# Optimization experiments

Hardware: AMD Instinct MI355X
Metric: run time of the kernel (lower is better)

Reference implementation:

```python
import jax, jax.numpy as jnp
import numpy as np

N = 100000   # nodes of target type
N1 = 80000   # nodes of second type
D = 128      # raw feature dim
H = 64       # hidden dim
C = 16       # n_classes
G = 3        # number of graphs (metapaths)
E = 1000000  # edges per graph
K = 20       # neighbors per node for NS branch
LP_LAYERS = 3


def setup_inputs() -> dict:
    key = jax.random.key(0)
    ks = jax.random.split(key, 24)
    f = lambda i, shape: jax.random.normal(ks[i], shape, dtype=jnp.float32)
    feats0 = f(0, (N, D))
    feats1 = f(1, (N1, D))
    W0 = f(2, (D, H)) * 0.05
    b0 = jnp.zeros((H,), jnp.float32)
    W1 = f(3, (D, H)) * 0.05
    b1 = jnp.zeros((H,), jnp.float32)
    Wp = f(4, (D, H)) * 0.05
    Wcls = f(5, (H, C)) * 0.05
    bcls = jnp.zeros((C,), jnp.float32)
    alpha = f(6, (N, 1)) * 0.1
    attention = f(7, (N, G, 1))
    y = jax.random.randint(ks[8], (N,), 0, C)
    labels_one_hot = jax.nn.one_hot(y, C, dtype=jnp.float32)
    byte_idx_train = jax.random.bernoulli(ks[9], 0.3, (N, 1))
    label_init = jnp.full((N, C), 1.0 / C, jnp.float32)
    nei_idx = jax.random.randint(ks[10], (N, K), 0, N1, dtype=jnp.int32)
    src0 = jax.random.randint(ks[11], (E,), 0, N, dtype=jnp.int32)
    dst0 = jax.random.randint(ks[12], (E,), 0, N, dtype=jnp.int32)
    src1 = jax.random.randint(ks[13], (E,), 0, N, dtype=jnp.int32)
    dst1 = jax.random.randint(ks[14], (E,), 0, N, dtype=jnp.int32)
    src2 = jax.random.randint(ks[15], (E,), 0, N, dtype=jnp.int32)
    dst2 = jax.random.randint(ks[16], (E,), 0, N, dtype=jnp.int32)
    return dict(feats0=feats0, feats1=feats1, W0=W0, b0=b0, W1=W1, b1=b1,
                Wp=Wp, Wcls=Wcls, bcls=bcls, alpha=alpha, attention=attention,
                labels_one_hot=labels_one_hot, label_init=label_init,
                byte_idx_train=byte_idx_train, nei_idx=nei_idx,
                src0=src0, dst0=dst0, src1=src1, dst1=dst1, src2=src2, dst2=dst2)


def _propagate(fp, h, src, dst, n):
    # edge attention: dot-product score of projected feats, softmax per dst
    s = jnp.sum(fp[src] * fp[dst], axis=-1) / np.sqrt(fp.shape[-1])   # [E]
    m = jax.ops.segment_max(s, dst, num_segments=n)                   # [N]
    e = jnp.exp(s - jnp.where(jnp.isfinite(m), m, 0.0)[dst])          # [E]
    denom = jax.ops.segment_sum(e, dst, num_segments=n)               # [N]
    att = e / (denom[dst] + 1e-16)                                    # [E]
    return jax.ops.segment_sum(att[:, None] * h[src], dst, num_segments=n)


def reference(feats0, feats1, W0, b0, W1, b1, Wp, Wcls, bcls, alpha, attention,
              labels_one_hot, label_init, byte_idx_train, nei_idx,
              src0, dst0, src1, dst1, src2, dst2):
    n = label_init.shape[0]
    masked = byte_idx_train.astype(jnp.float32)          # [N,1]
    masked_label = 1.0 - masked                          # (~mask).float()
    masked_onehot = labels_one_hot * masked              # clamp train labels

    fp = feats0 @ Wp                                     # shared projected feats [N,H]
    h_prime = []
    for src, dst in ((src0, dst0), (src1, dst1), (src2, dst2)):
        h = label_init
        for _ in range(LP_LAYERS):
            h = _propagate(fp, h, src, dst, n)
            h = h * masked_label + masked_onehot
        h_prime.append(h)
    x = jnp.stack(h_prime, axis=-1)                      # [N, C, G]
    att_g = jax.nn.softmax(attention, axis=1)            # [N, G, 1]
    logits_lp = jnp.matmul(x, att_g).squeeze(-1)         # [N, C]

    # NS_ec branch: per-type projection + neighbor-mean aggregation + classifier
    h0 = feats0 @ W0 + b0                                # [N, H]
    h1 = feats1 @ W1 + b1                                # [N1, H]
    z = h0 + jnp.mean(h1[nei_idx], axis=1)               # [N, H]
    logits_ns = z @ Wcls + bcls                          # [N, C]

    gate = jax.nn.sigmoid(alpha)
    logits = gate * logits_lp + jax.nn.sigmoid(-alpha) * logits_ns
    return logits, logits_lp, logits_ns
```

## Files before the change

### kernel.cpp

```cpp
#include <hip/hip_runtime.h>
#include <stdint.h>
#include <stddef.h>

__device__ __forceinline__ float bl(unsigned u){ return __uint_as_float(u << 16); }
__device__ __forceinline__ float bh(unsigned u){ return __uint_as_float(u & 0xffff0000u); }
__device__ __forceinline__ unsigned short f2bf(float f){
    unsigned u = __float_as_uint(f);
    unsigned r = (u + 0x7fffu + ((u >> 16) & 1u)) >> 16;
    return (unsigned short)r;
}
__device__ __forceinline__ void ntstore_u2(uint2* p, unsigned x, unsigned y){
    unsigned long long v = ((unsigned long long)y << 32) | (unsigned long long)x;
    __builtin_nontemporal_store(v, (unsigned long long*)p);
}

__global__ void detect_kernel(const unsigned char* __restrict__ mp, int n,
                              const unsigned* __restrict__ li, long li_n,
                              unsigned* __restrict__ flags){
    long i = (long)blockIdx.x*blockDim.x + threadIdx.x;
    unsigned f = 0;
    if(i < n){
        unsigned char b = mp[i];
        if((i & 3) && b) f |= 1u;
        if(b == 0x3Fu)   f |= 2u;
    }
    if(i < li_n){
        if(li[i] != li[0]) f |= 4u;
    }
    if(f) atomicOr(flags, f);
}
__device__ __forceinline__ float get_mask(const void* p, unsigned flags, int i){
    if((flags & 1u) == 0) return ((const int*)p)[i] ? 1.0f : 0.0f;
    if(flags & 2u)        return ((const float*)p)[i];
    return ((const unsigned char*)p)[i] ? 1.0f : 0.0f;
}

__global__ void small_w_kernel(const float* __restrict__ W0, const float* __restrict__ b0,
                               const float* __restrict__ W1, const float* __restrict__ b1,
                               const float* __restrict__ Wcls, const float* __restrict__ bcls,
                               float* __restrict__ W0c, float* __restrict__ W1c,
                               float* __restrict__ b0c, float* __restrict__ b1c)
{
    int t = threadIdx.x;
    for(int i = t; i < 2048; i += 256){
        int d = i >> 4, c = i & 15;
        float s0 = 0.f, s1 = 0.f;
        for(int k = 0; k < 64; k++){
            float wc = Wcls[k*16 + c];
            s0 += W0[d*64 + k]*wc;
            s1 += W1[d*64 + k]*wc;
        }
        W0c[i] = s0; W1c[i] = s1;
    }
    if(t < 16){
        float s0 = 0.f, s1 = 0.f;
        for(int k = 0; k < 64; k++){
            float wc = Wcls[k*16 + t];
            s0 += b0[k]*wc; s1 += b1[k]*wc;
        }
        b0c[t] = s0 + bcls[t];
        b1c[t] = s1;
    }
}

__global__ __launch_bounds__(256) void proj_fused0(
    const float* __restrict__ X, const float* __restrict__ Wp,
    const float* __restrict__ W0c, const float* __restrict__ b0c,
    unsigned short* __restrict__ fph, float* __restrict__ h0c, int rows)
{
    __shared__ float Wl[128*64];
    __shared__ float Wcl[128*16];
    __shared__ float ftile[32*128];
    int t = threadIdx.x;
    for(int i = t; i < 2048; i += 256) ((float4*)Wl)[i]  = ((const float4*)Wp)[i];
    for(int i = t; i < 512;  i += 256) ((float4*)Wcl)[i] = ((const float4*)W0c)[i];
    int c4 = (t & 15)*4;
    int col16 = t & 15;
    int r2 = (t >> 4)*2;
    float bc = b0c[col16];
    for(long base = (long)blockIdx.x*32; base < rows; base += (long)gridDim.x*32){
        int nr = min(32, (int)(rows - base));
        __syncthreads();
        for(int i = t; i < nr*32; i += 256){
            int r = i >> 5, q = i & 31;
            ((float4*)ftile)[r*32 + q] = ((const float4*)X)[(base + r)*32 + q];
        }
        __syncthreads();
        float a00=0,a01=0,a02=0,a03=0, a10=0,a11=0,a12=0,a13=0;
        float c0 = bc, c1 = bc;
        #pragma unroll 4
        for(int k = 0; k < 128; k++){
            float4 w = *((const float4*)(Wl + k*64 + c4));
            float wc = Wcl[k*16 + col16];
            float x0 = ftile[r2*128 + k];
            float x1 = ftile[(r2+1)*128 + k];
            a00 += x0*w.x; a01 += x0*w.y; a02 += x0*w.z; a03 += x0*w.w; c0 += x0*wc;
            a10 += x1*w.x; a11 += x1*w.y; a12 += x1*w.z; a13 += x1*w.w; c1 += x1*wc;
        }
        if(r2 < nr){
            ushort4 o; o.x=f2bf(a00); o.y=f2bf(a01); o.z=f2bf(a02); o.w=f2bf(a03);
            *((ushort4*)(fph + (base + r2)*64 + c4)) = o;
            h0c[(base + r2)*16 + col16] = c0;
        }
        if(r2 + 1 < nr){
            ushort4 o; o.x=f2bf(a10); o.y=f2bf(a11); o.z=f2bf(a12); o.w=f2bf(a13);
            *((ushort4*)(fph + (base + r2 + 1)*64 + c4)) = o;
            h0c[(base + r2 + 1)*16 + col16] = c1;
        }
    }
}

__global__ __launch_bounds__(256) void proj16_kernel(
    const float* __restrict__ X, const float* __restrict__ Wc,
    const float* __restrict__ biasc, unsigned short* __restrict__ Y, int rows)
{
    __shared__ float Wcl[128*16];
    __shared__ float ftile[64*128];
    int t = threadIdx.x;
    for(int i = t; i < 512; i += 256) ((float4*)Wcl)[i] = ((const float4*)Wc)[i];
    int col = t & 15;
    int r4 = (t >> 4)*4;
    float bc = biasc[col];
    for(long base = (long)blockIdx.x*64; base < rows; base += (long)gridDim.x*64){
        int nr = min(64, (int)(rows - base));
        __syncthreads();
        for(int i = t; i < nr*32; i += 256){
            int r = i >> 5, q = i & 31;
            ((float4*)ftile)[r*32 + q] = ((const float4*)X)[(base + r)*32 + q];
        }
        __syncthreads();
        float acc0 = bc, acc1 = bc, acc2 = bc, acc3 = bc;
        #pragma unroll 4
        for(int k = 0; k < 128; k++){
            float wc = Wcl[k*16 + col];
            acc0 += ftile[(r4+0)*128 + k]*wc;
            acc1 += ftile[(r4+1)*128 + k]*wc;
            acc2 += ftile[(r4+2)*128 + k]*wc;
            acc3 += ftile[(r4+3)*128 + k]*wc;
        }
        if(r4+0 < nr) Y[(base + r4 + 0)*16 + col] = f2bf(acc0);
        if(r4+1 < nr) Y[(base + r4 + 1)*16 + col] = f2bf(acc1);
        if(r4+2 < nr) Y[(base + r4 + 2)*16 + col] = f2bf(acc2);
        if(r4+3 < nr) Y[(base + r4 + 3)*16 + col] = f2bf(acc3);
    }
}

__global__ __launch_bounds__(256) void count_kernel(
    const int* __restrict__ dst0, const int* __restrict__ dst1, const int* __restrict__ dst2,
    int* __restrict__ deg, int n, int eg)
{
    long tid = (long)blockIdx.x*blockDim.x + threadIdx.x;
    if(tid >= 3L*eg) return;
    int g = (int)(tid / eg);
    int e = (int)(tid - (long)g*eg);
    const int* dp = g==0 ? dst0 : (g==1 ? dst1 : dst2);
    atomicAdd(&deg[(long)g*n + dp[e]], 1);
}

__global__ __launch_bounds__(256) void scanA_kernel(const int* __restrict__ deg,
                                                    int* __restrict__ incl,
                                                    int* __restrict__ bsum, int n3)
{
    __shared__ int sh[256];
    int t = threadIdx.x;
    long base = (long)blockIdx.x*1024 + t*4;
    int v0=0,v1=0,v2=0,v3=0;
    if(base   < n3) v0 = deg[base];
    if(base+1 < n3) v1 = deg[base+1];
    if(base+2 < n3) v2 = deg[base+2];
    if(base+3 < n3) v3 = deg[base+3];
    int tot = v0+v1+v2+v3;
    sh[t] = tot;
    __syncthreads();
    for(int ofs = 1; ofs < 256; ofs <<= 1){
        int add = (t >= ofs) ? sh[t-ofs] : 0;
        __syncthreads();
        sh[t] += add;
        __syncthreads();
    }
    int pre = sh[t] - tot;
    if(t == 255) bsum[blockIdx.x] = sh[255];
    int s0 = pre+v0, s1 = s0+v1, s2 = s1+v2, s3 = s2+v3;
    if(base   < n3) incl[base]   = s0;
    if(base+1 < n3) incl[base+1] = s1;
    if(base+2 < n3) incl[base+2] = s2;
    if(base+3 < n3) incl[base+3] = s3;
}

__global__ __launch_bounds__(512) void scanB_kernel(int* __restrict__ bsum, int nb)
{
    __shared__ int sh[512];
    int t = threadIdx.x;
    int v = (t < nb) ? bsum[t] : 0;
    sh[t] = v;
    __syncthreads();
    for(int ofs = 1; ofs < 512; ofs <<= 1){
        int add = (t >= ofs) ? sh[t-ofs] : 0;
        __syncthreads();
        sh[t] += add;
        __syncthreads();
    }
    if(t < nb) bsum[t] = sh[t] - v;
}

__global__ __launch_bounds__(256) void scanC_kernel(const int* __restrict__ incl,
                                                    const int* __restrict__ boff,
                                                    int* __restrict__ rowptr,
                                                    int* __restrict__ cursor, int n3)
{
    int i = blockIdx.x*blockDim.x + threadIdx.x;
    if(i >= n3) return;
    int ex = (i == 0) ? 0 : (incl[i-1] + boff[(i-1) >> 10]);
    rowptr[i] = ex;
    cursor[i] = ex;
    if(i == n3-1) rowptr[n3] = incl[i] + boff[i >> 10];
}

__global__ __launch_bounds__(256) void score_scatter_packed(
    const unsigned short* __restrict__ fph,
    const int* __restrict__ src0, const int* __restrict__ dst0,
    const int* __restrict__ src1, const int* __restrict__ dst1,
    const int* __restrict__ src2, const int* __restrict__ dst2,
    int* __restrict__ cursor, uint2* __restrict__ rec, int n, int eg)
{
    long tid = (long)blockIdx.x*blockDim.x + threadIdx.x;
    long gid = tid >> 3;
    long tot = 3L*eg;
    long e0 = gid*4;
    if(e0 >= tot) return;
    int l = threadIdx.x & 7;
    const uint4* f4 = (const uint4*)fph;

    int sv[4], dv[4], gv[4];
    bool ok[4];
    #pragma unroll
    for(int q = 0; q < 4; q++){
        long e = e0 + q;
        ok[q] = (e < tot);
        long ee = ok[q] ? e : (tot - 1);
        int g = (int)(ee / eg);
        int i = (int)(ee - (long)g*eg);
        const int* sp = g==0 ? src0 : (g==1 ? src1 : src2);
        const int* dp = g==0 ? dst0 : (g==1 ? dst1 : dst2);
        sv[q] = sp[i];
        dv[q] = dp[i];
        gv[q] = g;
    }
    uint4 A[4], B[4];
    #pragma unroll
    for(int q = 0; q < 4; q++){
        A[q] = f4[(long)sv[q]*8 + l];
        B[q] = f4[(long)dv[q]*8 + l];
    }
    float p[4];
    #pragma unroll
    for(int q = 0; q < 4; q++){
        float v;
        v  = bl(A[q].x)*bl(B[q].x) + bh(A[q].x)*bh(B[q].x);
        v += bl(A[q].y)*bl(B[q].y) + bh(A[q].y)*bh(B[q].y);
        v += bl(A[q].z)*bl(B[q].z) + bh(A[q].z)*bh(B[q].z);
        v += bl(A[q].w)*bl(B[q].w) + bh(A[q].w)*bh(B[q].w);
        p[q] = v;
    }
    #pragma unroll
    for(int q = 0; q < 4; q++){
        p[q] += __shfl_xor(p[q], 1);
        p[q] += __shfl_xor(p[q], 2);
        p[q] += __shfl_xor(p[q], 4);
    }
    if(l == 0){
        int pos[4];
        #pragma unroll
        for(int q = 0; q < 4; q++){
            if(ok[q]) pos[q] = atomicAdd(&cursor[(long)gv[q]*n + dv[q]], 1);
        }
        #pragma unroll
        for(int q = 0; q < 4; q++){
            if(ok[q]){
                float ev = __expf(fminf(p[q]*0.125f, 70.0f));
                ntstore_u2(&rec[pos[q]], (unsigned)sv[q], __float_as_uint(ev));
            }
        }
    }
}

template<int L1>
__global__ __launch_bounds__(256) void propagate_rec_kernel(
    const int* __restrict__ rowptr, const uint2* __restrict__ rec,
    const float* __restrict__ h_in_f32, const unsigned short* __restrict__ h_in_bf,
    unsigned short* __restrict__ h_next, const float* __restrict__ labels,
    const void* __restrict__ maskp, const unsigned* __restrict__ flags, int n)
{
    long tid = (long)blockIdx.x*blockDim.x + threadIdx.x;
    int row = (int)(tid >> 2);
    int c4 = (int)(tid & 3)*4;
    if(row >= 3*n) return;
    int g = row / n;
    int d = row - g*n;
    int beg = rowptr[row], end = rowptr[row+1];
    unsigned fl = *flags;
    float a0=0.f, a1=0.f, a2=0.f, a3=0.f;
    if(L1 && !(fl & 4u)){
        float v = (end > beg) ? h_in_f32[0] : 0.f;
        a0 = a1 = a2 = a3 = v;
    } else if(L1){
        float den = 0.f;
        for(int j = beg; j < end; j++){
            uint2 r = rec[j];
            float e = __uint_as_float(r.y);
            den += e;
            float4 hv = *((const float4*)(h_in_f32 + (long)r.x*16 + c4));
            a0 += e*hv.x; a1 += e*hv.y; a2 += e*hv.z; a3 += e*hv.w;
        }
        float inv = 1.0f/(den + 1e-16f);
        a0 *= inv; a1 *= inv; a2 *= inv; a3 *= inv;
    } else {
        const unsigned short* hg = h_in_bf + (long)g*n*16;
        float den = 0.f;
        int j = beg;
        if((j & 1) && j < end){
            uint2 r = rec[j];
            float e = __uint_as_float(r.y);
            den += e;
            uint2 hv = *((const uint2*)(hg + (long)r.x*16 + c4));
            a0 += e*bl(hv.x); a1 += e*bh(hv.x); a2 += e*bl(hv.y); a3 += e*bh(hv.y);
            j++;
        }
        for(; j + 1 < end; j += 2){
            uint4 rr = *((const uint4*)(&rec[j]));
            float e0 = __uint_as_float(rr.y);
            float e1 = __uint_as_float(rr.w);
            den += e0 + e1;
            uint2 hv0 = *((const uint2*)(hg + (long)rr.x*16 + c4));
            uint2 hv1 = *((const uint2*)(hg + (long)rr.z*16 + c4));
            a0 += e0*bl(hv0.x) + e1*bl(hv1.x);
            a1 += e0*bh(hv0.x) + e1*bh(hv1.x);
            a2 += e0*bl(hv0.y) + e1*bl(hv1.y);
            a3 += e0*bh(hv0.y) + e1*bh(hv1.y);
        }
        if(j < end){
            uint2 r = rec[j];
            float e = __uint_as_float(r.y);
            den += e;
            uint2 hv = *((const uint2*)(hg + (long)r.x*16 + c4));
            a0 += e*bl(hv.x); a1 += e*bh(hv.x); a2 += e*bl(hv.y); a3 += e*bh(hv.y);
        }
        float inv = 1.0f/(den + 1e-16f);
        a0 *= inv; a1 *= inv; a2 *= inv; a3 *= inv;
    }
    float mk = get_mask(maskp, fl, d);
    float im = 1.0f - mk;
    float4 lb = *((const float4*)(labels + (long)d*16 + c4));
    ushort4 o;
    o.x = f2bf(a0*im + lb.x*mk);
    o.y = f2bf(a1*im + lb.y*mk);
    o.z = f2bf(a2*im + lb.z*mk);
    o.w = f2bf(a3*im + lb.w*mk);
    *((ushort4*)(h_next + (long)row*16 + c4)) = o;
}

__global__ __launch_bounds__(256) void ns_final_kernel(
    const unsigned short* __restrict__ hf, const float* __restrict__ h0c,
    const unsigned short* __restrict__ h1c, const int* __restrict__ nei,
    const float* __restrict__ attn, const float* __restrict__ alpha,
    float* __restrict__ out, int n, int kk)
{
    long tid = (long)blockIdx.x*blockDim.x + threadIdx.x;
    int node = (int)(tid >> 2);
    int c4 = (int)(tid & 3)*4;
    if(node >= n) return;
    const int* nrow = nei + (long)node*kk;
    float s0=0.f, s1=0.f, s2=0.f, s3=0.f;
    for(int j = 0; j < kk; j++){
        int nb = nrow[j];
        uint2 hv = *((const uint2*)(h1c + (long)nb*16 + c4));
        s0 += bl(hv.x); s1 += bh(hv.x); s2 += bl(hv.y); s3 += bh(hv.y);
    }
    float invk = 1.0f/(float)kk;
    float4 h0 = *((const float4*)(h0c + (long)node*16 + c4));
    float ns0 = h0.x + s0*invk, ns1 = h0.y + s1*invk;
    float ns2 = h0.z + s2*invk, ns3 = h0.w + s3*invk;
    float a0 = attn[node*3], a1 = attn[node*3+1], a2 = attn[node*3+2];
    float mx = fmaxf(a0, fmaxf(a1, a2));
    float e0 = __expf(a0-mx), e1 = __expf(a1-mx), e2 = __expf(a2-mx);
    float inv = 1.0f/(e0+e1+e2);
    e0 *= inv; e1 *= inv; e2 *= inv;
    long gs = (long)n*16;
    long idx = (long)node*16 + c4;
    uint2 f0 = *((const uint2*)(hf + idx));
    uint2 f1 = *((const uint2*)(hf + gs + idx));
    uint2 f2v = *((const uint2*)(hf + 2*gs + idx));
    float lp0 = e0*bl(f0.x) + e1*bl(f1.x) + e2*bl(f2v.x);
    float lp1 = e0*bh(f0.x) + e1*bh(f1.x) + e2*bh(f2v.x);
    float lp2 = e0*bl(f0.y) + e1*bl(f1.y) + e2*bl(f2v.y);
    float lp3 = e0*bh(f0.y) + e1*bh(f1.y) + e2*bh(f2v.y);
    float al = alpha[node];
    float sg = 1.0f/(1.0f + __expf(-al));
    float isg = 1.0f - sg;
    float4 o0; o0.x = sg*lp0 + isg*ns0; o0.y = sg*lp1 + isg*ns1;
               o0.z = sg*lp2 + isg*ns2; o0.w = sg*lp3 + isg*ns3;
    float4 o1; o1.x = lp0; o1.y = lp1; o1.z = lp2; o1.w = lp3;
    float4 o2; o2.x = ns0; o2.y = ns1; o2.z = ns2; o2.w = ns3;
    *((float4*)(out + idx))        = o0;
    *((float4*)(out + gs + idx))   = o1;
    *((float4*)(out + 2*gs + idx)) = o2;
}

extern "C" void kernel_launch(void* const* d_in, const int* in_sizes, int n_in,
                              void* d_out, int out_size, void* d_ws, size_t ws_size,
                              hipStream_t stream)
{
    const float* feats0     = (const float*)d_in[0];
    const float* feats1     = (const float*)d_in[1];
    const float* W0         = (const float*)d_in[2];
    const float* b0         = (const float*)d_in[3];
    const float* W1         = (const float*)d_in[4];
    const float* b1         = (const float*)d_in[5];
    const float* Wp         = (const float*)d_in[6];
    const float* Wcls       = (const float*)d_in[7];
    const float* bcls       = (const float*)d_in[8];
    const float* alpha      = (const float*)d_in[9];
    const float* attn       = (const float*)d_in[10];
    const float* labels     = (const float*)d_in[11];
    const float* label_init = (const float*)d_in[12];
    const void*  maskp      = d_in[13];
    const int*   nei        = (const int*)d_in[14];
    const int*   src0       = (const int*)d_in[15];
    const int*   dst0       = (const int*)d_in[16];
    const int*   src1       = (const int*)d_in[17];
    const int*   dst1       = (const int*)d_in[18];
    const int*   src2       = (const int*)d_in[19];
    const int*   dst2       = (const int*)d_in[20];

    const int n  = in_sizes[9];
    const int n1 = in_sizes[1] / 128;
    const int eg = in_sizes[15];
    const int kk = in_sizes[14] / n;
    const int n3 = 3*n;

    char* ws = (char*)d_ws;
    size_t off = 0;
    auto alloc = [&](size_t bytes)->char*{
        char* p = ws + off; off += (bytes + 255) & ~(size_t)255; return p;
    };
    unsigned*       flags  = (unsigned*)      alloc(256);
    unsigned short* fph    = (unsigned short*)alloc((size_t)n*64*2);
    float*          h0c    = (float*)         alloc((size_t)n*16*4);
    unsigned short* h1c    = (unsigned short*)alloc((size_t)n1*16*2);
    float*          W0c    = (float*)         alloc(2048*4);
    float*          W1c    = (float*)         alloc(2048*4);
    float*          b0c    = (float*)         alloc(64);
    float*          b1c    = (float*)         alloc(64);
    int*            deg    = (int*)           alloc((size_t)n3*4);
    int*            cursor = (int*)           alloc((size_t)n3*4);
    int*            bsum   = (int*)           alloc(512*4);
    int*            rowptr = (int*)           alloc(((size_t)n3+1)*4);
    uint2*          rec    = (uint2*)         alloc((size_t)3*eg*8);
    unsigned short* hA     = (unsigned short*)alloc((size_t)n3*16*2);
    unsigned short* hB     = (unsigned short*)alloc((size_t)n3*16*2);
    int* incl = deg;

    hipMemsetAsync(flags, 0, 4, stream);
    hipMemsetAsync(deg, 0, (size_t)n3*4, stream);
    {
        long li_n = (long)n*16;
        detect_kernel<<<(unsigned)((li_n+255)/256), 256, 0, stream>>>(
            (const unsigned char*)maskp, n, (const unsigned*)label_init, li_n, flags);
    }

    small_w_kernel<<<1, 256, 0, stream>>>(W0, b0, W1, b1, Wcls, bcls, W0c, W1c, b0c, b1c);

    proj_fused0<<<(n+31)/32, 256, 0, stream>>>(feats0, Wp, W0c, b0c, fph, h0c, n);
    proj16_kernel<<<(n1+63)/64, 256, 0, stream>>>(feats1, W1c, b1c, h1c, n1);

    {
        long tot = 3L*eg;
        count_kernel<<<(unsigned)((tot+255)/256), 256, 0, stream>>>(dst0, dst1, dst2, deg, n, eg);
    }
    int nb = (n3 + 1023)/1024;
    scanA_kernel<<<nb, 256, 0, stream>>>(deg, incl, bsum, n3);
    scanB_kernel<<<1, 512, 0, stream>>>(bsum, nb);
    scanC_kernel<<<(n3+255)/256, 256, 0, stream>>>(incl, bsum, rowptr, cursor, n3);

    {
        long groups = (3L*eg + 3)/4;
        long tthreads = groups*8;
        score_scatter_packed<<<(unsigned)((tthreads+255)/256), 256, 0, stream>>>(
            fph, src0,dst0,src1,dst1,src2,dst2, cursor, rec, n, eg);
    }

    {
        long tot = (long)n3*4;
        unsigned gsz = (unsigned)((tot+255)/256);
        propagate_rec_kernel<1><<<gsz, 256, 0, stream>>>(
            rowptr, rec, label_init, nullptr, hA, labels, maskp, flags, n);
        propagate_rec_kernel<0><<<gsz, 256, 0, stream>>>(
            rowptr, rec, nullptr, hA, hB, labels, maskp, flags, n);
        propagate_rec_kernel<0><<<gsz, 256, 0, stream>>>(
            rowptr, rec, nullptr, hB, hA, labels, maskp, flags, n);
    }

    ns_final_kernel<<<(unsigned)(((long)n*4+255)/256), 256, 0, stream>>>(
        hA, h0c, h1c, nei, attn, alpha, (float*)d_out, n, kk);
}
```

Measured before the change: 506.8 us.

## Fuse prep kernels, merge proj16 with degree count, fold last propagate into final

The mask/label detect kernel is merged with the small weight-fold kernel into one launch, and the feats1 projection shares a launch with the edge degree count through block-index partitioning. The third label-propagation layer is fused into the final NS/combine kernel, so each node thread walks all three graphs' rows, applies the label clamp and the attention softmax in registers, and skips the round trip of the last bf16 h buffer. This cuts launch count and one full read/write of the propagated state. The trade-off is that the final kernel now does three irregular row traversals per thread, which may lower its occupancy and increase per-thread latency.

```diff
diff --git a/kernel.cpp b/kernel.cpp
--- a/kernel.cpp
+++ b/kernel.cpp
@@ -13,53 +13,54 @@
     unsigned long long v = ((unsigned long long)y << 32) | (unsigned long long)x;
     __builtin_nontemporal_store(v, (unsigned long long*)p);
 }
-
-__global__ void detect_kernel(const unsigned char* __restrict__ mp, int n,
-                              const unsigned* __restrict__ li, long li_n,
-                              unsigned* __restrict__ flags){
-    long i = (long)blockIdx.x*blockDim.x + threadIdx.x;
-    unsigned f = 0;
-    if(i < n){
-        unsigned char b = mp[i];
-        if((i & 3) && b) f |= 1u;
-        if(b == 0x3Fu)   f |= 2u;
-    }
-    if(i < li_n){
-        if(li[i] != li[0]) f |= 4u;
-    }
-    if(f) atomicOr(flags, f);
-}
 __device__ __forceinline__ float get_mask(const void* p, unsigned flags, int i){
     if((flags & 1u) == 0) return ((const int*)p)[i] ? 1.0f : 0.0f;
     if(flags & 2u)        return ((const float*)p)[i];
     return ((const unsigned char*)p)[i] ? 1.0f : 0.0f;
 }
 
-__global__ void small_w_kernel(const float* __restrict__ W0, const float* __restrict__ b0,
-                               const float* __restrict__ W1, const float* __restrict__ b1,
-                               const float* __restrict__ Wcls, const float* __restrict__ bcls,
-                               float* __restrict__ W0c, float* __restrict__ W1c,
-                               float* __restrict__ b0c, float* __restrict__ b1c)
+__global__ __launch_bounds__(256) void prep_kernel(
+    const float* __restrict__ W0, const float* __restrict__ b0,
+    const float* __restrict__ W1, const float* __restrict__ b1,
+    const float* __restrict__ Wcls, const float* __restrict__ bcls,
+    float* __restrict__ W0c, float* __restrict__ W1c,
+    float* __restrict__ b0c, float* __restrict__ b1c,
+    const unsigned char* __restrict__ mp, int n,
+    const unsigned* __restrict__ li, long li_n, unsigned* __restrict__ flags)
 {
     int t = threadIdx.x;
-    for(int i = t; i < 2048; i += 256){
-        int d = i >> 4, c = i & 15;
-        float s0 = 0.f, s1 = 0.f;
-        for(int k = 0; k < 64; k++){
-            float wc = Wcls[k*16 + c];
-            s0 += W0[d*64 + k]*wc;
-            s1 += W1[d*64 + k]*wc;
-        }
-        W0c[i] = s0; W1c[i] = s1;
-    }
-    if(t < 16){
-        float s0 = 0.f, s1 = 0.f;
-        for(int k = 0; k < 64; k++){
-            float wc = Wcls[k*16 + t];
-            s0 += b0[k]*wc; s1 += b1[k]*wc;
-        }
-        b0c[t] = s0 + bcls[t];
-        b1c[t] = s1;
+    if(blockIdx.x == 0){
+        for(int i = t; i < 2048; i += 256){
+            int d = i >> 4, c = i & 15;
+            float s0 = 0.f, s1 = 0.f;
+            for(int k = 0; k < 64; k++){
+                float wc = Wcls[k*16 + c];
+                s0 += W0[d*64 + k]*wc;
+                s1 += W1[d*64 + k]*wc;
+            }
+            W0c[i] = s0; W1c[i] = s1;
+        }
+        if(t < 16){
+            float s0 = 0.f, s1 = 0.f;
+            for(int k = 0; k < 64; k++){
+                float wc = Wcls[k*16 + t];
+                s0 += b0[k]*wc; s1 += b1[k]*wc;
+            }
+            b0c[t] = s0 + bcls[t];
+            b1c[t] = s1;
+        }
+    } else {
+        long i = (long)(blockIdx.x - 1)*256 + t;
+        unsigned f = 0;
+        if(i < n){
+            unsigned char b = mp[i];
+            if((i & 3) && b) f |= 1u;
+            if(b == 0x3Fu)   f |= 2u;
+        }
+        if(i < li_n){
+            if(li[i] != li[0]) f |= 4u;
+        }
+        if(f) atomicOr(flags, f);
     }
 }
 
@@ -110,51 +111,53 @@
     }
 }
 
-__global__ __launch_bounds__(256) void proj16_kernel(
+__global__ __launch_bounds__(256) void proj16_count_kernel(
     const float* __restrict__ X, const float* __restrict__ Wc,
-    const float* __restrict__ biasc, unsigned short* __restrict__ Y, int rows)
+    const float* __restrict__ biasc, unsigned short* __restrict__ Y, int rows,
+    int nbProj,
+    const int* __restrict__ dst0, const int* __restrict__ dst1, const int* __restrict__ dst2,
+    int* __restrict__ deg, int n, int eg)
 {
     __shared__ float Wcl[128*16];
     __shared__ float ftile[64*128];
     int t = threadIdx.x;
-    for(int i = t; i < 512; i += 256) ((float4*)Wcl)[i] = ((const float4*)Wc)[i];
-    int col = t & 15;
-    int r4 = (t >> 4)*4;
-    float bc = biasc[col];
-    for(long base = (long)blockIdx.x*64; base < rows; base += (long)gridDim.x*64){
-        int nr = min(64, (int)(rows - base));
-        __syncthreads();
-        for(int i = t; i < nr*32; i += 256){
-            int r = i >> 5, q = i & 31;
-            ((float4*)ftile)[r*32 + q] = ((const float4*)X)[(base + r)*32 + q];
-        }
-        __syncthreads();
-        float acc0 = bc, acc1 = bc, acc2 = bc, acc3 = bc;
-        #pragma unroll 4
-        for(int k = 0; k < 128; k++){
-            float wc = Wcl[k*16 + col];
-            acc0 += ftile[(r4+0)*128 + k]*wc;
-            acc1 += ftile[(r4+1)*128 + k]*wc;
-            acc2 += ftile[(r4+2)*128 + k]*wc;
-            acc3 += ftile[(r4+3)*128 + k]*wc;
-        }
-        if(r4+0 < nr) Y[(base + r4 + 0)*16 + col] = f2bf(acc0);
-        if(r4+1 < nr) Y[(base + r4 + 1)*16 + col] = f2bf(acc1);
-        if(r4+2 < nr) Y[(base + r4 + 2)*16 + col] = f2bf(acc2);
-        if(r4+3 < nr) Y[(base + r4 + 3)*16 + col] = f2bf(acc3);
-    }
-}
-
-__global__ __launch_bounds__(256) void count_kernel(
-    const int* __restrict__ dst0, const int* __restrict__ dst1, const int* __restrict__ dst2,
-    int* __restrict__ deg, int n, int eg)
-{
-    long tid = (long)blockIdx.x*blockDim.x + threadIdx.x;
-    if(tid >= 3L*eg) return;
-    int g = (int)(tid / eg);
-    int e = (int)(tid - (long)g*eg);
-    const int* dp = g==0 ? dst0 : (g==1 ? dst1 : dst2);
-    atomicAdd(&deg[(long)g*n + dp[e]], 1);
+    if(blockIdx.x < nbProj){
+        for(int i = t; i < 512; i += 256) ((float4*)Wcl)[i] = ((const float4*)Wc)[i];
+        int col = t & 15;
+        int r4 = (t >> 4)*4;
+        float bc = biasc[col];
+        long base = (long)blockIdx.x*64;
+        if(base < rows){
+            int nr = min(64, (int)(rows - base));
+            __syncthreads();
+            for(int i = t; i < nr*32; i += 256){
+                int r = i >> 5, q = i & 31;
+                ((float4*)ftile)[r*32 + q] = ((const float4*)X)[(base + r)*32 + q];
+            }
+            __syncthreads();
+            float acc0 = bc, acc1 = bc, acc2 = bc, acc3 = bc;
+            #pragma unroll 4
+            for(int k = 0; k < 128; k++){
+                float wc = Wcl[k*16 + col];
+                acc0 += ftile[(r4+0)*128 + k]*wc;
+                acc1 += ftile[(r4+1)*128 + k]*wc;
+                acc2 += ftile[(r4+2)*128 + k]*wc;
+                acc3 += ftile[(r4+3)*128 + k]*wc;
+            }
+            if(r4+0 < nr) Y[(base + r4 + 0)*16 + col] = f2bf(acc0);
+            if(r4+1 < nr) Y[(base + r4 + 1)*16 + col] = f2bf(acc1);
+            if(r4+2 < nr) Y[(base + r4 + 2)*16 + col] = f2bf(acc2);
+            if(r4+3 < nr) Y[(base + r4 + 3)*16 + col] = f2bf(acc3);
+        }
+    } else {
+        long tid = (long)(blockIdx.x - nbProj)*256 + t;
+        if(tid < 3L*eg){
+            int g = (int)(tid / eg);
+            int e = (int)(tid - (long)g*eg);
+            const int* dp = g==0 ? dst0 : (g==1 ? dst1 : dst2);
+            atomicAdd(&deg[(long)g*n + dp[e]], 1);
+        }
+    }
 }
 
 __global__ __launch_bounds__(256) void scanA_kernel(const int* __restrict__ deg,
@@ -282,6 +285,45 @@
             }
         }
     }
+}
+
+__device__ __forceinline__ void prop_row_bf16(
+    const uint2* __restrict__ rec, int beg, int end,
+    const unsigned short* __restrict__ hg, int c4,
+    float &a0, float &a1, float &a2, float &a3)
+{
+    float den = 0.f;
+    a0 = a1 = a2 = a3 = 0.f;
+    int j = beg;
+    if((j & 1) && j < end){
+        uint2 r = rec[j];
+        float e = __uint_as_float(r.y);
+        den += e;
+        uint2 hv = *((const uint2*)(hg + (long)r.x*16 + c4));
+        a0 += e*bl(hv.x); a1 += e*bh(hv.x); a2 += e*bl(hv.y); a3 += e*bh(hv.y);
+        j++;
+    }
+    for(; j + 1 < end; j += 2){
+        uint4 rr = *((const uint4*)(&rec[j]));
+        float e0 = __uint_as_float(rr.y);
+        float e1 = __uint_as_float(rr.w);
+        den += e0 + e1;
+        uint2 hv0 = *((const uint2*)(hg + (long)rr.x*16 + c4));
+        uint2 hv1 = *((const uint2*)(hg + (long)rr.z*16 + c4));
+        a0 += e0*bl(hv0.x) + e1*bl(hv1.x);
+        a1 += e0*bh(hv0.x) + e1*bh(hv1.x);
+        a2 += e0*bl(hv0.y) + e1*bl(hv1.y);
+        a3 += e0*bh(hv0.y) + e1*bh(hv1.y);
+    }
+    if(j < end){
+        uint2 r = rec[j];
+        float e = __uint_as_float(r.y);
+        den += e;
+        uint2 hv = *((const uint2*)(hg + (long)r.x*16 + c4));
+        a0 += e*bl(hv.x); a1 += e*bh(hv.x); a2 += e*bl(hv.y); a3 += e*bh(hv.y);
+    }
+    float inv = 1.0f/(den + 1e-16f);
+    a0 *= inv; a1 *= inv; a2 *= inv; a3 *= inv;
 }
 
 template<int L1>
@@ -315,38 +357,7 @@
         float inv = 1.0f/(den + 1e-16f);
         a0 *= inv; a1 *= inv; a2 *= inv; a3 *= inv;
     } else {
-        const unsigned short* hg = h_in_bf + (long)g*n*16;
-        float den = 0.f;
-        int j = beg;
-        if((j & 1) && j < end){
-            uint2 r = rec[j];
-            float e = __uint_as_float(r.y);
-            den += e;
-            uint2 hv = *((const uint2*)(hg + (long)r.x*16 + c4));
-            a0 += e*bl(hv.x); a1 += e*bh(hv.x); a2 += e*bl(hv.y); a3 += e*bh(hv.y);
-            j++;
-        }
-        for(; j + 1 < end; j += 2){
-            uint4 rr = *((const uint4*)(&rec[j]));
-            float e0 = __uint_as_float(rr.y);
-            float e1 = __uint_as_float(rr.w);
-            den += e0 + e1;
-            uint2 hv0 = *((const uint2*)(hg + (long)rr.x*16 + c4));
-            uint2 hv1 = *((const uint2*)(hg + (long)rr.z*16 + c4));
-            a0 += e0*bl(hv0.x) + e1*bl(hv1.x);
-            a1 += e0*bh(hv0.x) + e1*bh(hv1.x);
-            a2 += e0*bl(hv0.y) + e1*bl(hv1.y);
-            a3 += e0*bh(hv0.y) + e1*bh(hv1.y);
-        }
-        if(j < end){
-            uint2 r = rec[j];
-            float e = __uint_as_float(r.y);
-            den += e;
-            uint2 hv = *((const uint2*)(hg + (long)r.x*16 + c4));
-            a0 += e*bl(hv.x); a1 += e*bh(hv.x); a2 += e*bl(hv.y); a3 += e*bh(hv.y);
-        }
-        float inv = 1.0f/(den + 1e-16f);
-        a0 *= inv; a1 *= inv; a2 *= inv; a3 *= inv;
+        prop_row_bf16(rec, beg, end, h_in_bf + (long)g*n*16, c4, a0, a1, a2, a3);
     }
     float mk = get_mask(maskp, fl, d);
     float im = 1.0f - mk;
@@ -359,16 +370,45 @@
     *((ushort4*)(h_next + (long)row*16 + c4)) = o;
 }
 
-__global__ __launch_bounds__(256) void ns_final_kernel(
-    const unsigned short* __restrict__ hf, const float* __restrict__ h0c,
-    const unsigned short* __restrict__ h1c, const int* __restrict__ nei,
-    const float* __restrict__ attn, const float* __restrict__ alpha,
-    float* __restrict__ out, int n, int kk)
+__global__ __launch_bounds__(256) void prop3_ns_kernel(
+    const int* __restrict__ rowptr, const uint2* __restrict__ rec,
+    const unsigned short* __restrict__ h_in_bf, const float* __restrict__ labels,
+    const void* __restrict__ maskp, const unsigned* __restrict__ flags,
+    const float* __restrict__ h0c, const unsigned short* __restrict__ h1c,
+    const int* __restrict__ nei, const float* __restrict__ attn,
+    const float* __restrict__ alpha, float* __restrict__ out, int n, int kk)
 {
     long tid = (long)blockIdx.x*blockDim.x + threadIdx.x;
     int node = (int)(tid >> 2);
     int c4 = (int)(tid & 3)*4;
     if(node >= n) return;
+    unsigned fl = *flags;
+    float mk = get_mask(maskp, fl, node);
+    float im = 1.0f - mk;
+    float4 lb = *((const float4*)(labels + (long)node*16 + c4));
+
+    float lp_[3][4];
+    #pragma unroll
+    for(int g = 0; g < 3; g++){
+        int row = g*n + node;
+        float a0, a1, a2, a3;
+        prop_row_bf16(rec, rowptr[row], rowptr[row+1], h_in_bf + (long)g*n*16, c4,
+                      a0, a1, a2, a3);
+        lp_[g][0] = a0*im + lb.x*mk;
+        lp_[g][1] = a1*im + lb.y*mk;
+        lp_[g][2] = a2*im + lb.z*mk;
+        lp_[g][3] = a3*im + lb.w*mk;
+    }
+    float t0 = attn[node*3], t1 = attn[node*3+1], t2 = attn[node*3+2];
+    float mx = fmaxf(t0, fmaxf(t1, t2));
+    float e0 = __expf(t0-mx), e1 = __expf(t1-mx), e2 = __expf(t2-mx);
+    float inv = 1.0f/(e0+e1+e2);
+    e0 *= inv; e1 *= inv; e2 *= inv;
+    float lp0 = e0*lp_[0][0] + e1*lp_[1][0] + e2*lp_[2][0];
+    float lp1 = e0*lp_[0][1] + e1*lp_[1][1] + e2*lp_[2][1];
+    float lp2 = e0*lp_[0][2] + e1*lp_[1][2] + e2*lp_[2][2];
+    float lp3 = e0*lp_[0][3] + e1*lp_[1][3] + e2*lp_[2][3];
+
     const int* nrow = nei + (long)node*kk;
     float s0=0.f, s1=0.f, s2=0.f, s3=0.f;
     for(int j = 0; j < kk; j++){
@@ -380,23 +420,12 @@
     float4 h0 = *((const float4*)(h0c + (long)node*16 + c4));
     float ns0 = h0.x + s0*invk, ns1 = h0.y + s1*invk;
     float ns2 = h0.z + s2*invk, ns3 = h0.w + s3*invk;
-    float a0 = attn[node*3], a1 = attn[node*3+1], a2 = attn[node*3+2];
-    float mx = fmaxf(a0, fmaxf(a1, a2));
-    float e0 = __expf(a0-mx), e1 = __expf(a1-mx), e2 = __expf(a2-mx);
-    float inv = 1.0f/(e0+e1+e2);
-    e0 *= inv; e1 *= inv; e2 *= inv;
-    long gs = (long)n*16;
-    long idx = (long)node*16 + c4;
-    uint2 f0 = *((const uint2*)(hf + idx));
-    uint2 f1 = *((const uint2*)(hf + gs + idx));
-    uint2 f2v = *((const uint2*)(hf + 2*gs + idx));
-    float lp0 = e0*bl(f0.x) + e1*bl(f1.x) + e2*bl(f2v.x);
-    float lp1 = e0*bh(f0.x) + e1*bh(f1.x) + e2*bh(f2v.x);
-    float lp2 = e0*bl(f0.y) + e1*bl(f1.y) + e2*bl(f2v.y);
-    float lp3 = e0*bh(f0.y) + e1*bh(f1.y) + e2*bh(f2v.y);
+
     float al = alpha[node];
     float sg = 1.0f/(1.0f + __expf(-al));
     float isg = 1.0f - sg;
+    long gs = (long)n*16;
+    long idx = (long)node*16 + c4;
     float4 o0; o0.x = sg*lp0 + isg*ns0; o0.y = sg*lp1 + isg*ns1;
                o0.z = sg*lp2 + isg*ns2; o0.w = sg*lp3 + isg*ns3;
     float4 o1; o1.x = lp0; o1.y = lp1; o1.z = lp2; o1.w = lp3;
@@ -462,21 +491,25 @@
 
     hipMemsetAsync(flags, 0, 4, stream);
     hipMemsetAsync(deg, 0, (size_t)n3*4, stream);
+
     {
         long li_n = (long)n*16;
-        detect_kernel<<<(unsigned)((li_n+255)/256), 256, 0, stream>>>(
-            (const unsigned char*)maskp, n, (const unsigned*)label_init, li_n, flags);
-    }
-
-    small_w_kernel<<<1, 256, 0, stream>>>(W0, b0, W1, b1, Wcls, bcls, W0c, W1c, b0c, b1c);
+        unsigned gsz = 1 + (unsigned)((li_n + 255)/256);
+        prep_kernel<<<gsz, 256, 0, stream>>>(W0, b0, W1, b1, Wcls, bcls,
+                                             W0c, W1c, b0c, b1c,
+                                             (const unsigned char*)maskp, n,
+                                             (const unsigned*)label_init, li_n, flags);
+    }
 
     proj_fused0<<<(n+31)/32, 256, 0, stream>>>(feats0, Wp, W0c, b0c, fph, h0c, n);
-    proj16_kernel<<<(n1+63)/64, 256, 0, stream>>>(feats1, W1c, b1c, h1c, n1);
-
     {
+        int nbProj = (n1 + 63)/64;
         long tot = 3L*eg;
-        count_kernel<<<(unsigned)((tot+255)/256), 256, 0, stream>>>(dst0, dst1, dst2, deg, n, eg);
-    }
+        unsigned nbCount = (unsigned)((tot + 255)/256);
+        proj16_count_kernel<<<nbProj + nbCount, 256, 0, stream>>>(
+            feats1, W1c, b1c, h1c, n1, nbProj, dst0, dst1, dst2, deg, n, eg);
+    }
+
     int nb = (n3 + 1023)/1024;
     scanA_kernel<<<nb, 256, 0, stream>>>(deg, incl, bsum, n3);
     scanB_kernel<<<1, 512, 0, stream>>>(bsum, nb);
@@ -496,10 +529,9 @@
             rowptr, rec, label_init, nullptr, hA, labels, maskp, flags, n);
         propagate_rec_kernel<0><<<gsz, 256, 0, stream>>>(
             rowptr, rec, nullptr, hA, hB, labels, maskp, flags, n);
-        propagate_rec_kernel<0><<<gsz, 256, 0, stream>>>(
-            rowptr, rec, nullptr, hB, hA, labels, maskp, flags, n);
-    }
-
-    ns_final_kernel<<<(unsigned)(((long)n*4+255)/256), 256, 0, stream>>>(
-        hA, h0c, h1c, nei, attn, alpha, (float*)d_out, n, kk);
-}
+    }
+
+    prop3_ns_kernel<<<(unsigned)(((long)n*4+255)/256), 256, 0, stream>>>(
+        rowptr, rec, hB, labels, maskp, flags, h0c, h1c, nei, attn, alpha,
+        (float*)d_out, n, kk);
+}
```

Measured after the change: 485.1 us. 4.3% less time.
